# Kernel tuning notes

Measured on AMD Instinct MI355X. Metric: run time of the kernel, lower is better.

The kernel has to match this reference:

```python
import jax, jax.numpy as jnp
import numpy as np

N = 50000
E = 800000
IN_DIM = 128
HID = 128
OUT = 40


def setup_inputs() -> dict:
    key = jax.random.key(0)
    k1, k2, k3, k4, k5 = jax.random.split(key, 5)
    x = jax.random.normal(k1, (N, IN_DIM), dtype=jnp.float32)
    edge_index = jax.random.randint(k2, (2, E), 0, N, dtype=jnp.int64)
    # Glorot-ish init for GCNConv weights, zero bias (PyG default bias=True)
    W1 = jax.random.normal(k3, (IN_DIM, HID), dtype=jnp.float32) / np.sqrt(IN_DIM)
    b1 = jnp.zeros((HID,), dtype=jnp.float32)
    W2 = jax.random.normal(k4, (HID, OUT), dtype=jnp.float32) / np.sqrt(HID)
    b2 = jnp.zeros((OUT,), dtype=jnp.float32)
    return {"x": x, "edge_index": edge_index, "W1": W1, "b1": b1, "W2": W2, "b2": b2}


def _gcn_norm(edge_index, n_nodes):
    """Add self-loops and compute symmetric GCN normalization per edge.
    Returns (src, dst, norm) with len E + n_nodes."""
    loops = jnp.arange(n_nodes, dtype=edge_index.dtype)
    src = jnp.concatenate([edge_index[0], loops])
    dst = jnpp_concat = jnp.concatenate([edge_index[1], loops])
    dst = jnp.concatenate([edge_index[1], loops])
    deg = jax.ops.segment_sum(jnp.ones_like(dst, dtype=jnp.float32), dst,
                              num_segments=n_nodes)
    dinv = jnp.where(deg > 0, jax.lax.rsqrt(deg), 0.0)
    norm = dinv[src] * dinv[dst]  # [E + N]
    return src, dst, norm


def _gcn_conv(x, src, dst, norm, W, b, n_nodes):
    xw = x @ W                                  # [N, F_out] transform first
    msg = xw[src] * norm[:, None]               # gather + scale, [E+N, F_out]
    out = jax.ops.segment_sum(msg, dst, num_segments=n_nodes)  # scatter-add
    return out + b


def reference(x, edge_index, W1, b1, W2, b2):
    n = x.shape[0]
    src, dst, norm = _gcn_norm(edge_index, n)
    h = _gcn_conv(x, src, dst, norm, W1, b1, n)
    h = jax.nn.relu(h)
    # dropout is identity in eval mode (training=False)
    h = _gcn_conv(h, src, dst, norm, W2, b2, n)
    return jax.nn.softmax(h, axis=1)
```

## Files before the change

kernel.cpp:

```cpp
#include <hip/hip_runtime.h>
#include <hip/hip_fp16.h>

#define IN_DIM 128
#define HID    128
#define OUTC   40
#define CAP    64
#define LSTR   136

typedef _Float16 f16x8 __attribute__((ext_vector_type(8)));
typedef _Float16 f16x4 __attribute__((ext_vector_type(4)));
typedef float    f32x4 __attribute__((ext_vector_type(4)));

__device__ __forceinline__ int permi(int d, int NP8) { return (d & 7) * NP8 + (d >> 3); }

__global__ __launch_bounds__(256) void k_scatter(const int* __restrict__ edge, int* __restrict__ cnt,
                                                 int* __restrict__ col,
                                                 const float* __restrict__ W1, const float* __restrict__ W2,
                                                 _Float16* __restrict__ W1T, _Float16* __restrict__ W2T,
                                                 int E, int n, int nbS, int NP8) {
  int b = blockIdx.x;
  if (b >= nbS) {
    int t = (b - nbS) * 256 + threadIdx.x;
    if (t < 128 * 128) {
      int nn = t >> 7, kk = t & 127;
      W1T[t] = (_Float16)W1[kk * 128 + nn];
    }
    if (t < 48 * 128) {
      int nn = t >> 7, kk = t & 127;
      W2T[t] = (nn < OUTC) ? (_Float16)W2[kk * OUTC + nn] : (_Float16)0.f;
    }
    return;
  }
  int g       = b & 7;
  int tid     = (b >> 3) * 256 + threadIdx.x;
  int gstride = (nbS >> 3) * 256;
  for (int e = tid; e < E; e += gstride) {
    int d = edge[E + e];
    if ((unsigned)d >= (unsigned)n || (d & 7) != g) continue;
    int sv = edge[e];
    if ((unsigned)sv >= (unsigned)n) continue;
    int p   = g * NP8 + (d >> 3);
    int pos = atomicAdd(&cnt[p], 1);
    if (pos < CAP) col[(size_t)p * CAP + pos] = sv;
  }
}


__global__ __launch_bounds__(256) void k_gemm1(const float* __restrict__ x, const _Float16* __restrict__ W1T,
                                               const int* __restrict__ cnt, __half* __restrict__ out,
                                               int n, int NP8) {
  __shared__ _Float16 sW[128 * LSTR];
  __shared__ _Float16 sX[64 * LSTR];
  int tid = threadIdx.x;
  int i0  = blockIdx.x * 64;

  {
    const uint4* src = (const uint4*)W1T;
    for (int idx = tid; idx < 2048; idx += 256) {
      int nn = idx >> 4, c = idx & 15;
      *(uint4*)&sW[nn * LSTR + c * 8] = src[nn * 16 + c];
    }
  }
  for (int idx = tid; idx < 2048; idx += 256) {
    int r = idx >> 5, c = idx & 31;
    int row = i0 + r;
    float4 v = (row < n) ? *(const float4*)&x[(size_t)row * IN_DIM + c * 4]
                         : make_float4(0.f, 0.f, 0.f, 0.f);
    f16x4 hv; hv[0] = (_Float16)v.x; hv[1] = (_Float16)v.y; hv[2] = (_Float16)v.z; hv[3] = (_Float16)v.w;
    *(f16x4*)&sX[r * LSTR + c * 4] = hv;
  }
  __syncthreads();

  int wv = tid >> 6, lane = tid & 63;
  int m = lane & 15, quad = lane >> 4;

  const _Float16* ax = &sX[(16 * wv + m) * LSTR + quad * 8];
  f16x8 a0 = *(const f16x8*)(ax);
  f16x8 a1 = *(const f16x8*)(ax + 32);
  f16x8 a2 = *(const f16x8*)(ax + 64);
  f16x8 a3 = *(const f16x8*)(ax + 96);

  int base_row = i0 + 16 * wv + quad * 4;
  float dvr[4];
#pragma unroll
  for (int r = 0; r < 4; ++r) {
    int row = base_row + r;
    dvr[r] = (row < n) ? rsqrtf((float)(cnt[permi(row, NP8)] + 1)) : 0.f;
  }

#pragma unroll
  for (int t = 0; t < 8; ++t) {
    const _Float16* bx = &sW[(t * 16 + m) * LSTR + quad * 8];
    f16x8 b0 = *(const f16x8*)(bx);
    f16x8 b1 = *(const f16x8*)(bx + 32);
    f16x8 b2 = *(const f16x8*)(bx + 64);
    f16x8 b3 = *(const f16x8*)(bx + 96);
    f32x4 c = {0.f, 0.f, 0.f, 0.f};
    c = __builtin_amdgcn_mfma_f32_16x16x32_f16(a0, b0, c, 0, 0, 0);
    c = __builtin_amdgcn_mfma_f32_16x16x32_f16(a1, b1, c, 0, 0, 0);
    c = __builtin_amdgcn_mfma_f32_16x16x32_f16(a2, b2, c, 0, 0, 0);
    c = __builtin_amdgcn_mfma_f32_16x16x32_f16(a3, b3, c, 0, 0, 0);
    int colb = t * 16 + m;
#pragma unroll
    for (int r = 0; r < 4; ++r) {
      int row = base_row + r;
      if (row < n) out[(size_t)row * HID + colb] = __float2half(c[r] * dvr[r]);
    }
  }
}


__global__ __launch_bounds__(256) void k_agg1(const __half2* __restrict__ xws, const int* __restrict__ cnt,
                                              const int* __restrict__ col, const float* __restrict__ b1,
                                              __half2* __restrict__ h, int n, int NP8) {
  int wid  = (blockIdx.x * 256 + threadIdx.x) >> 6;
  int lane = threadIdx.x & 63;
  if (wid >= n) return;
  float2 acc = __half22float2(xws[(size_t)wid * 64 + lane]);
  int p   = permi(wid, NP8);
  int deg = cnt[p];
  int end = min(deg, CAP);
  const int* cp = &col[(size_t)p * CAP];
  int e = 0;
  for (; e + 8 <= end; e += 8) {
    int s0 = cp[e], s1 = cp[e+1], s2 = cp[e+2], s3 = cp[e+3];
    int s4 = cp[e+4], s5 = cp[e+5], s6 = cp[e+6], s7 = cp[e+7];
    float2 v0 = __half22float2(xws[(size_t)s0 * 64 + lane]);
    float2 v1 = __half22float2(xws[(size_t)s1 * 64 + lane]);
    float2 v2 = __half22float2(xws[(size_t)s2 * 64 + lane]);
    float2 v3 = __half22float2(xws[(size_t)s3 * 64 + lane]);
    float2 v4 = __half22float2(xws[(size_t)s4 * 64 + lane]);
    float2 v5 = __half22float2(xws[(size_t)s5 * 64 + lane]);
    float2 v6 = __half22float2(xws[(size_t)s6 * 64 + lane]);
    float2 v7 = __half22float2(xws[(size_t)s7 * 64 + lane]);
    acc.x += (v0.x + v1.x) + (v2.x + v3.x) + ((v4.x + v5.x) + (v6.x + v7.x));
    acc.y += (v0.y + v1.y) + (v2.y + v3.y) + ((v4.y + v5.y) + (v6.y + v7.y));
  }
  for (; e < end; ++e) {
    float2 v = __half22float2(xws[(size_t)cp[e] * 64 + lane]);
    acc.x += v.x; acc.y += v.y;
  }
  float dv = rsqrtf((float)(deg + 1));
  float2 bb = ((const float2*)b1)[lane];
  h[(size_t)wid * 64 + lane] =
      __floats2half2_rn(fmaxf(acc.x * dv + bb.x, 0.f), fmaxf(acc.y * dv + bb.y, 0.f));
}


__global__ __launch_bounds__(256) void k_gemm2(const __half* __restrict__ h, const _Float16* __restrict__ W2T,
                                               const int* __restrict__ cnt, __half* __restrict__ out,
                                               int n, int NP8) {
  __shared__ _Float16 sW[48 * LSTR];
  __shared__ _Float16 sH[64 * LSTR];
  int tid = threadIdx.x;
  int i0  = blockIdx.x * 64;

  {
    const uint4* src = (const uint4*)W2T;
    for (int idx = tid; idx < 768; idx += 256) {
      int nn = idx >> 4, c = idx & 15;
      *(uint4*)&sW[nn * LSTR + c * 8] = src[nn * 16 + c];
    }
  }
  {
    const uint4* src = (const uint4*)h;
    for (int idx = tid; idx < 1024; idx += 256) {
      int r = idx >> 4, c = idx & 15;
      int row = i0 + r;
      uint4 v = (row < n) ? src[(size_t)row * 16 + c] : make_uint4(0u, 0u, 0u, 0u);
      *(uint4*)&sH[r * LSTR + c * 8] = v;
    }
  }
  __syncthreads();

  int wv = tid >> 6, lane = tid & 63;
  int m = lane & 15, quad = lane >> 4;

  const _Float16* ax = &sH[(16 * wv + m) * LSTR + quad * 8];
  f16x8 a0 = *(const f16x8*)(ax);
  f16x8 a1 = *(const f16x8*)(ax + 32);
  f16x8 a2 = *(const f16x8*)(ax + 64);
  f16x8 a3 = *(const f16x8*)(ax + 96);

  int base_row = i0 + 16 * wv + quad * 4;
  float dvr[4];
#pragma unroll
  for (int r = 0; r < 4; ++r) {
    int row = base_row + r;
    dvr[r] = (row < n) ? rsqrtf((float)(cnt[permi(row, NP8)] + 1)) : 0.f;
  }

#pragma unroll
  for (int t = 0; t < 3; ++t) {
    const _Float16* bx = &sW[(t * 16 + m) * LSTR + quad * 8];
    f16x8 b0 = *(const f16x8*)(bx);
    f16x8 b1 = *(const f16x8*)(bx + 32);
    f16x8 b2 = *(const f16x8*)(bx + 64);
    f16x8 b3 = *(const f16x8*)(bx + 96);
    f32x4 c = {0.f, 0.f, 0.f, 0.f};
    c = __builtin_amdgcn_mfma_f32_16x16x32_f16(a0, b0, c, 0, 0, 0);
    c = __builtin_amdgcn_mfma_f32_16x16x32_f16(a1, b1, c, 0, 0, 0);
    c = __builtin_amdgcn_mfma_f32_16x16x32_f16(a2, b2, c, 0, 0, 0);
    c = __builtin_amdgcn_mfma_f32_16x16x32_f16(a3, b3, c, 0, 0, 0);
    int colb = t * 16 + m;
    if (colb < OUTC) {
#pragma unroll
      for (int r = 0; r < 4; ++r) {
        int row = base_row + r;
        if (row < n) out[(size_t)row * OUTC + colb] = __float2half(c[r] * dvr[r]);
      }
    }
  }
}


__global__ __launch_bounds__(256) void k_agg2(const __half* __restrict__ hw, const int* __restrict__ cnt,
                                              const int* __restrict__ col, const float* __restrict__ b2,
                                              float* __restrict__ out, int n, int NP8) {
  int wid  = (blockIdx.x * 256 + threadIdx.x) >> 6;
  int lane = threadIdx.x & 63;
  if (wid >= n) return;
  bool act = lane < OUTC;
  int li = act ? lane : 0;
  float acc = act ? __half2float(hw[(size_t)wid * OUTC + li]) : 0.f;
  int p   = permi(wid, NP8);
  int deg = cnt[p];
  int end = min(deg, CAP);
  const int* cp = &col[(size_t)p * CAP];
  int e = 0;
  for (; e + 8 <= end; e += 8) {
    int s0 = cp[e], s1 = cp[e+1], s2 = cp[e+2], s3 = cp[e+3];
    int s4 = cp[e+4], s5 = cp[e+5], s6 = cp[e+6], s7 = cp[e+7];
    if (act) {
      float a0 = __half2float(hw[(size_t)s0 * OUTC + li]);
      float a1 = __half2float(hw[(size_t)s1 * OUTC + li]);
      float a2 = __half2float(hw[(size_t)s2 * OUTC + li]);
      float a3 = __half2float(hw[(size_t)s3 * OUTC + li]);
      float a4 = __half2float(hw[(size_t)s4 * OUTC + li]);
      float a5 = __half2float(hw[(size_t)s5 * OUTC + li]);
      float a6 = __half2float(hw[(size_t)s6 * OUTC + li]);
      float a7 = __half2float(hw[(size_t)s7 * OUTC + li]);
      acc += (a0 + a1) + (a2 + a3) + ((a4 + a5) + (a6 + a7));
    }
  }
  for (; e < end; ++e) {
    int s = cp[e];
    if (act) acc += __half2float(hw[(size_t)s * OUTC + li]);
  }
  float logit = acc * rsqrtf((float)(deg + 1)) + (act ? b2[lane] : 0.f);
  float m = act ? logit : -1e30f;
#pragma unroll
  for (int o = 32; o > 0; o >>= 1) m = fmaxf(m, __shfl_xor(m, o, 64));
  float ex = act ? __expf(logit - m) : 0.f;
  float sum = ex;
#pragma unroll
  for (int o = 32; o > 0; o >>= 1) sum += __shfl_xor(sum, o, 64);
  if (act) out[(size_t)wid * OUTC + lane] = ex / sum;
}


extern "C" void kernel_launch(void* const* d_in, const int* in_sizes, int n_in,
                              void* d_out, int out_size, void* d_ws, size_t ws_size,
                              hipStream_t stream) {
  const float* x    = (const float*)d_in[0];
  const int*   edge = (const int*)d_in[1];
  const float* W1   = (const float*)d_in[2];
  const float* b1   = (const float*)d_in[3];
  const float* W2   = (const float*)d_in[4];
  const float* b2   = (const float*)d_in[5];
  float* out = (float*)d_out;

  int N   = in_sizes[0] / IN_DIM;
  int E   = in_sizes[1] / 2;
  int NP8 = (N + 7) / 8;
  int NP  = NP8 * 8;

  char* ws = (char*)d_ws;
  size_t off = 0;
  auto carve = [&](size_t bytes) { char* p = ws + off; off = (off + bytes + 255) & ~(size_t)255; return p; };
  int*      cnt = (int*)carve((size_t)NP * 4);
  int*      col = (int*)carve((size_t)NP * CAP * 4);
  _Float16* W1T = (_Float16*)carve((size_t)128 * 128 * 2);
  _Float16* W2T = (_Float16*)carve((size_t)48 * 128 * 2);
  __half*   xws = (__half*)carve((size_t)N * HID * 2);
  __half*   h   = (__half*)carve((size_t)N * HID * 2);
  __half*   hw  = xws;

  hipMemsetAsync(cnt, 0, (size_t)NP * 4, stream);

  int nbS = 1024;
  k_scatter<<<nbS + 64, 256, 0, stream>>>(edge, cnt, col, W1, W2, W1T, W2T, E, N, nbS, NP8);

  k_gemm1<<<(N + 63) / 64, 256, 0, stream>>>(x, W1T, cnt, xws, N, NP8);
  k_agg1<<<(N * 64 + 255) / 256, 256, 0, stream>>>((const __half2*)xws, cnt, col, b1, (__half2*)h, N, NP8);
  k_gemm2<<<(N + 63) / 64, 256, 0, stream>>>(h, W2T, cnt, hw, N, NP8);
  k_agg2<<<(N * 64 + 255) / 256, 256, 0, stream>>>(hw, cnt, col, b2, out, N, NP8);
}
```

Baseline: 220.1 us.

## Two-pass LDS-binned edge partition and 16-bit column indices

Replaces the single scatter kernel, where every block rescanned all edges and kept only one of eight destination groups, with two passes. The first pass bins each edge chunk by destination group in shared memory and flushes contiguous packed (dst>>3, src) words to per-group staging arrays. The second pass scatters from staging into the padded adjacency. Column indices shrink to 16-bit, which halves adjacency traffic in the aggregation kernels but only holds while N fits in 65536 nodes. The change costs an extra kernel launch and a staging buffer round trip.

New measurement: 222.5 us. No clear change (+1.1%).

```diff
diff --git a/kernel.cpp b/kernel.cpp
--- a/kernel.cpp
+++ b/kernel.cpp
@@ -6,6 +6,8 @@
 #define OUTC   40
 #define CAP    64
 #define LSTR   136
+#define CHUNK  4096
+#define BINCAP 800
 
 typedef _Float16 f16x8 __attribute__((ext_vector_type(8)));
 typedef _Float16 f16x4 __attribute__((ext_vector_type(4)));
@@ -13,14 +15,14 @@
 
 __device__ __forceinline__ int permi(int d, int NP8) { return (d & 7) * NP8 + (d >> 3); }
 
-__global__ __launch_bounds__(256) void k_scatter(const int* __restrict__ edge, int* __restrict__ cnt,
-                                                 int* __restrict__ col,
-                                                 const float* __restrict__ W1, const float* __restrict__ W2,
-                                                 _Float16* __restrict__ W1T, _Float16* __restrict__ W2T,
-                                                 int E, int n, int nbS, int NP8) {
+__global__ __launch_bounds__(256) void k_part(const int* __restrict__ edge, unsigned* __restrict__ staging,
+                                              int* __restrict__ gcnt,
+                                              const float* __restrict__ W1, const float* __restrict__ W2,
+                                              _Float16* __restrict__ W1T, _Float16* __restrict__ W2T,
+                                              int E, int n, int nbA, int ES8) {
   int b = blockIdx.x;
-  if (b >= nbS) {
-    int t = (b - nbS) * 256 + threadIdx.x;
+  if (b >= nbA) {
+    int t = (b - nbA) * 256 + threadIdx.x;
     if (t < 128 * 128) {
       int nn = t >> 7, kk = t & 127;
       W1T[t] = (_Float16)W1[kk * 128 + nn];
@@ -31,17 +33,56 @@
     }
     return;
   }
-  int g       = b & 7;
-  int tid     = (b >> 3) * 256 + threadIdx.x;
-  int gstride = (nbS >> 3) * 256;
-  for (int e = tid; e < E; e += gstride) {
-    int d = edge[E + e];
-    if ((unsigned)d >= (unsigned)n || (d & 7) != g) continue;
-    int sv = edge[e];
-    if ((unsigned)sv >= (unsigned)n) continue;
-    int p   = g * NP8 + (d >> 3);
+  __shared__ unsigned lbin[8][BINCAP];
+  __shared__ int lcnt[8];
+  __shared__ int lbase[8];
+  int tid = threadIdx.x;
+  if (tid < 8) lcnt[tid] = 0;
+  __syncthreads();
+  int e0 = b * CHUNK;
+#pragma unroll 4
+  for (int i = 0; i < CHUNK / 256; ++i) {
+    int e = e0 + i * 256 + tid;
+    if (e < E) {
+      int sv = edge[e];
+      int d  = edge[E + e];
+      if ((unsigned)d < (unsigned)n && (unsigned)sv < (unsigned)n) {
+        int g = d & 7;
+        unsigned pk = ((unsigned)(d >> 3) << 16) | (unsigned)sv;
+        int p = atomicAdd(&lcnt[g], 1);
+        if (p < BINCAP) lbin[g][p] = pk;
+        else {
+          int gp = atomicAdd(&gcnt[g], 1);
+          staging[(size_t)g * ES8 + gp] = pk;
+        }
+      }
+    }
+  }
+  __syncthreads();
+  if (tid < 8) lbase[tid] = atomicAdd(&gcnt[tid], min(lcnt[tid], BINCAP));
+  __syncthreads();
+#pragma unroll
+  for (int g = 0; g < 8; ++g) {
+    int c = min(lcnt[g], BINCAP);
+    int base = lbase[g];
+    for (int idx = tid; idx < c; idx += 256)
+      staging[(size_t)g * ES8 + base + idx] = lbin[g][idx];
+  }
+}
+
+__global__ __launch_bounds__(256) void k_scat(const unsigned* __restrict__ staging, const int* __restrict__ gcnt,
+                                              int* __restrict__ cnt, unsigned short* __restrict__ col,
+                                              int NP8, int ES8) {
+  int g = blockIdx.x & 7;
+  int cE = gcnt[g];
+  int t       = (blockIdx.x >> 3) * 256 + threadIdx.x;
+  int gstride = (gridDim.x >> 3) * 256;
+  const unsigned* sg = &staging[(size_t)g * ES8];
+  for (int i = t; i < cE; i += gstride) {
+    unsigned pk = sg[i];
+    int p = g * NP8 + (int)(pk >> 16);
     int pos = atomicAdd(&cnt[p], 1);
-    if (pos < CAP) col[(size_t)p * CAP + pos] = sv;
+    if (pos < CAP) col[(size_t)p * CAP + pos] = (unsigned short)(pk & 0xFFFFu);
   }
 }
 
@@ -111,7 +152,7 @@
 
 
 __global__ __launch_bounds__(256) void k_agg1(const __half2* __restrict__ xws, const int* __restrict__ cnt,
-                                              const int* __restrict__ col, const float* __restrict__ b1,
+                                              const unsigned short* __restrict__ col, const float* __restrict__ b1,
                                               __half2* __restrict__ h, int n, int NP8) {
   int wid  = (blockIdx.x * 256 + threadIdx.x) >> 6;
   int lane = threadIdx.x & 63;
@@ -120,7 +161,7 @@
   int p   = permi(wid, NP8);
   int deg = cnt[p];
   int end = min(deg, CAP);
-  const int* cp = &col[(size_t)p * CAP];
+  const unsigned short* cp = &col[(size_t)p * CAP];
   int e = 0;
   for (; e + 8 <= end; e += 8) {
     int s0 = cp[e], s1 = cp[e+1], s2 = cp[e+2], s3 = cp[e+3];
@@ -215,7 +256,7 @@
 
 
 __global__ __launch_bounds__(256) void k_agg2(const __half* __restrict__ hw, const int* __restrict__ cnt,
-                                              const int* __restrict__ col, const float* __restrict__ b2,
+                                              const unsigned short* __restrict__ col, const float* __restrict__ b2,
                                               float* __restrict__ out, int n, int NP8) {
   int wid  = (blockIdx.x * 256 + threadIdx.x) >> 6;
   int lane = threadIdx.x & 63;
@@ -226,7 +267,7 @@
   int p   = permi(wid, NP8);
   int deg = cnt[p];
   int end = min(deg, CAP);
-  const int* cp = &col[(size_t)p * CAP];
+  const unsigned short* cp = &col[(size_t)p * CAP];
   int e = 0;
   for (; e + 8 <= end; e += 8) {
     int s0 = cp[e], s1 = cp[e+1], s2 = cp[e+2], s3 = cp[e+3];
@@ -274,22 +315,26 @@
   int E   = in_sizes[1] / 2;
   int NP8 = (N + 7) / 8;
   int NP  = NP8 * 8;
+  int ES8 = E / 8 + 16384;
 
   char* ws = (char*)d_ws;
   size_t off = 0;
   auto carve = [&](size_t bytes) { char* p = ws + off; off = (off + bytes + 255) & ~(size_t)255; return p; };
-  int*      cnt = (int*)carve((size_t)NP * 4);
-  int*      col = (int*)carve((size_t)NP * CAP * 4);
-  _Float16* W1T = (_Float16*)carve((size_t)128 * 128 * 2);
-  _Float16* W2T = (_Float16*)carve((size_t)48 * 128 * 2);
-  __half*   xws = (__half*)carve((size_t)N * HID * 2);
-  __half*   h   = (__half*)carve((size_t)N * HID * 2);
-  __half*   hw  = xws;
-
-  hipMemsetAsync(cnt, 0, (size_t)NP * 4, stream);
-
-  int nbS = 1024;
-  k_scatter<<<nbS + 64, 256, 0, stream>>>(edge, cnt, col, W1, W2, W1T, W2T, E, N, nbS, NP8);
+  int*            gcnt    = (int*)carve(8 * 4);
+  int*            cnt     = (int*)carve((size_t)NP * 4);
+  unsigned*       staging = (unsigned*)carve((size_t)8 * ES8 * 4);
+  unsigned short* col     = (unsigned short*)carve((size_t)NP * CAP * 2);
+  _Float16*       W1T     = (_Float16*)carve((size_t)128 * 128 * 2);
+  _Float16*       W2T     = (_Float16*)carve((size_t)48 * 128 * 2);
+  __half*         xws     = (__half*)carve((size_t)N * HID * 2);
+  __half*         h       = (__half*)carve((size_t)N * HID * 2);
+  __half*         hw      = xws;
+
+  hipMemsetAsync(gcnt, 0, (size_t)((char*)staging - (char*)gcnt), stream);
+
+  int nbA = (E + CHUNK - 1) / CHUNK;
+  k_part<<<nbA + 64, 256, 0, stream>>>(edge, staging, gcnt, W1, W2, W1T, W2T, E, N, nbA, ES8);
+  k_scat<<<512, 256, 0, stream>>>(staging, gcnt, cnt, col, NP8, ES8);
 
   k_gemm1<<<(N + 63) / 64, 256, 0, stream>>>(x, W1T, cnt, xws, N, NP8);
   k_agg1<<<(N * 64 + 255) / 256, 256, 0, stream>>>((const __half2*)xws, cnt, col, b1, (__half2*)h, N, NP8);
```

## Split degree count from scatter and co-schedule scatter with first GEMM

Applied to the files above, without the earlier changes.

Degree counting moves into a separate prep kernel, so the first GEMM (which needs degrees for normalization) can run in the same launch as the column-list scatter, overlapping atomic-bound scatter work with MFMA work. Column indices are stored as 16-bit values to halve index traffic in both aggregations. The second aggregation now uses half2 loads and float2 stores across 20 lanes. This adds an extra kernel and a second counter array, and the 16-bit indices only hold for graphs with fewer than 65536 nodes.

Result: slower. 278.6 us (+26.6%).

```diff
diff --git a/kernel.cpp b/kernel.cpp
--- a/kernel.cpp
+++ b/kernel.cpp
@@ -13,46 +13,61 @@
 
 __device__ __forceinline__ int permi(int d, int NP8) { return (d & 7) * NP8 + (d >> 3); }
 
-__global__ __launch_bounds__(256) void k_scatter(const int* __restrict__ edge, int* __restrict__ cnt,
-                                                 int* __restrict__ col,
-                                                 const float* __restrict__ W1, const float* __restrict__ W2,
-                                                 _Float16* __restrict__ W1T, _Float16* __restrict__ W2T,
-                                                 int E, int n, int nbS, int NP8) {
+__global__ __launch_bounds__(256) void k_prep(const int* __restrict__ edge, int* __restrict__ cnt,
+                                              const float* __restrict__ W1, const float* __restrict__ W2,
+                                              _Float16* __restrict__ W1T, _Float16* __restrict__ W2T,
+                                              int E, int n, int nbC, int NP8) {
   int b = blockIdx.x;
-  if (b >= nbS) {
-    int t = (b - nbS) * 256 + threadIdx.x;
-    if (t < 128 * 128) {
-      int nn = t >> 7, kk = t & 127;
-      W1T[t] = (_Float16)W1[kk * 128 + nn];
-    }
-    if (t < 48 * 128) {
-      int nn = t >> 7, kk = t & 127;
-      W2T[t] = (nn < OUTC) ? (_Float16)W2[kk * OUTC + nn] : (_Float16)0.f;
+  if (b < nbC) {
+    int e      = b * 256 + threadIdx.x;
+    int stride = nbC * 256;
+    for (; e < E; e += stride) {
+      int d = __builtin_nontemporal_load(&edge[E + e]);
+      if ((unsigned)d < (unsigned)n) atomicAdd(&cnt[permi(d, NP8)], 1);
     }
     return;
   }
-  int g       = b & 7;
-  int tid     = (b >> 3) * 256 + threadIdx.x;
-  int gstride = (nbS >> 3) * 256;
-  for (int e = tid; e < E; e += gstride) {
-    int d = edge[E + e];
-    if ((unsigned)d >= (unsigned)n || (d & 7) != g) continue;
-    int sv = edge[e];
-    if ((unsigned)sv >= (unsigned)n) continue;
-    int p   = g * NP8 + (d >> 3);
-    int pos = atomicAdd(&cnt[p], 1);
-    if (pos < CAP) col[(size_t)p * CAP + pos] = sv;
-  }
-}
-
-
-__global__ __launch_bounds__(256) void k_gemm1(const float* __restrict__ x, const _Float16* __restrict__ W1T,
-                                               const int* __restrict__ cnt, __half* __restrict__ out,
-                                               int n, int NP8) {
-  __shared__ _Float16 sW[128 * LSTR];
-  __shared__ _Float16 sX[64 * LSTR];
+  int t = (b - nbC) * 256 + threadIdx.x;
+  if (t < 128 * 128) {
+    int nn = t >> 7, kk = t & 127;
+    W1T[t] = (_Float16)W1[kk * 128 + nn];
+  }
+  if (t < 48 * 128) {
+    int nn = t >> 7, kk = t & 127;
+    W2T[t] = (nn < OUTC) ? (_Float16)W2[kk * OUTC + nn] : (_Float16)0.f;
+  }
+}
+
+#define SMEM_SZ (128 * LSTR * 2 + 64 * LSTR * 2)
+
+__global__ __launch_bounds__(256) void k_scatter_gemm1(const int* __restrict__ edge, int* __restrict__ fill,
+                                                       unsigned short* __restrict__ col,
+                                                       const float* __restrict__ x, const _Float16* __restrict__ W1T,
+                                                       const int* __restrict__ cnt, __half* __restrict__ xws,
+                                                       int E, int n, int nbS, int NP8) {
+  __shared__ __align__(16) char smem[SMEM_SZ];
+  int b   = blockIdx.x;
   int tid = threadIdx.x;
-  int i0  = blockIdx.x * 64;
+
+  if (b < nbS) {
+    int g       = b & 7;
+    int t       = (b >> 3) * 256 + tid;
+    int gstride = (nbS >> 3) * 256;
+    for (int e = t; e < E; e += gstride) {
+      int d = __builtin_nontemporal_load(&edge[E + e]);
+      if ((unsigned)d >= (unsigned)n || (d & 7) != g) continue;
+      int sv = __builtin_nontemporal_load(&edge[e]);
+      if ((unsigned)sv >= (unsigned)n) continue;
+      int p   = g * NP8 + (d >> 3);
+      int pos = atomicAdd(&fill[p], 1);
+      if (pos < CAP) col[(size_t)p * CAP + pos] = (unsigned short)sv;
+    }
+    return;
+  }
+
+  _Float16* sW = (_Float16*)smem;
+  _Float16* sX = (_Float16*)(smem + 128 * LSTR * 2);
+  int i0 = (b - nbS) * 64;
 
   {
     const uint4* src = (const uint4*)W1T;
@@ -104,14 +119,14 @@
 #pragma unroll
     for (int r = 0; r < 4; ++r) {
       int row = base_row + r;
-      if (row < n) out[(size_t)row * HID + colb] = __float2half(c[r] * dvr[r]);
+      if (row < n) xws[(size_t)row * HID + colb] = __float2half(c[r] * dvr[r]);
     }
   }
 }
 
 
 __global__ __launch_bounds__(256) void k_agg1(const __half2* __restrict__ xws, const int* __restrict__ cnt,
-                                              const int* __restrict__ col, const float* __restrict__ b1,
+                                              const unsigned short* __restrict__ col, const float* __restrict__ b1,
                                               __half2* __restrict__ h, int n, int NP8) {
   int wid  = (blockIdx.x * 256 + threadIdx.x) >> 6;
   int lane = threadIdx.x & 63;
@@ -120,7 +135,7 @@
   int p   = permi(wid, NP8);
   int deg = cnt[p];
   int end = min(deg, CAP);
-  const int* cp = &col[(size_t)p * CAP];
+  const unsigned short* cp = &col[(size_t)p * CAP];
   int e = 0;
   for (; e + 8 <= end; e += 8) {
     int s0 = cp[e], s1 = cp[e+1], s2 = cp[e+2], s3 = cp[e+3];
@@ -214,48 +229,60 @@
 }
 
 
-__global__ __launch_bounds__(256) void k_agg2(const __half* __restrict__ hw, const int* __restrict__ cnt,
-                                              const int* __restrict__ col, const float* __restrict__ b2,
+__global__ __launch_bounds__(256) void k_agg2(const __half2* __restrict__ hw2, const int* __restrict__ cnt,
+                                              const unsigned short* __restrict__ col, const float* __restrict__ b2,
                                               float* __restrict__ out, int n, int NP8) {
   int wid  = (blockIdx.x * 256 + threadIdx.x) >> 6;
   int lane = threadIdx.x & 63;
   if (wid >= n) return;
-  bool act = lane < OUTC;
+  bool act = lane < (OUTC / 2);
   int li = act ? lane : 0;
-  float acc = act ? __half2float(hw[(size_t)wid * OUTC + li]) : 0.f;
+  float2 acc = __half22float2(hw2[(size_t)wid * (OUTC / 2) + li]);
+  if (!act) { acc.x = 0.f; acc.y = 0.f; }
   int p   = permi(wid, NP8);
   int deg = cnt[p];
   int end = min(deg, CAP);
-  const int* cp = &col[(size_t)p * CAP];
+  const unsigned short* cp = &col[(size_t)p * CAP];
   int e = 0;
   for (; e + 8 <= end; e += 8) {
     int s0 = cp[e], s1 = cp[e+1], s2 = cp[e+2], s3 = cp[e+3];
     int s4 = cp[e+4], s5 = cp[e+5], s6 = cp[e+6], s7 = cp[e+7];
     if (act) {
-      float a0 = __half2float(hw[(size_t)s0 * OUTC + li]);
-      float a1 = __half2float(hw[(size_t)s1 * OUTC + li]);
-      float a2 = __half2float(hw[(size_t)s2 * OUTC + li]);
-      float a3 = __half2float(hw[(size_t)s3 * OUTC + li]);
-      float a4 = __half2float(hw[(size_t)s4 * OUTC + li]);
-      float a5 = __half2float(hw[(size_t)s5 * OUTC + li]);
-      float a6 = __half2float(hw[(size_t)s6 * OUTC + li]);
-      float a7 = __half2float(hw[(size_t)s7 * OUTC + li]);
-      acc += (a0 + a1) + (a2 + a3) + ((a4 + a5) + (a6 + a7));
+      float2 v0 = __half22float2(hw2[(size_t)s0 * (OUTC / 2) + li]);
+      float2 v1 = __half22float2(hw2[(size_t)s1 * (OUTC / 2) + li]);
+      float2 v2 = __half22float2(hw2[(size_t)s2 * (OUTC / 2) + li]);
+      float2 v3 = __half22float2(hw2[(size_t)s3 * (OUTC / 2) + li]);
+      float2 v4 = __half22float2(hw2[(size_t)s4 * (OUTC / 2) + li]);
+      float2 v5 = __half22float2(hw2[(size_t)s5 * (OUTC / 2) + li]);
+      float2 v6 = __half22float2(hw2[(size_t)s6 * (OUTC / 2) + li]);
+      float2 v7 = __half22float2(hw2[(size_t)s7 * (OUTC / 2) + li]);
+      acc.x += (v0.x + v1.x) + (v2.x + v3.x) + ((v4.x + v5.x) + (v6.x + v7.x));
+      acc.y += (v0.y + v1.y) + (v2.y + v3.y) + ((v4.y + v5.y) + (v6.y + v7.y));
     }
   }
   for (; e < end; ++e) {
     int s = cp[e];
-    if (act) acc += __half2float(hw[(size_t)s * OUTC + li]);
-  }
-  float logit = acc * rsqrtf((float)(deg + 1)) + (act ? b2[lane] : 0.f);
-  float m = act ? logit : -1e30f;
+    if (act) {
+      float2 v = __half22float2(hw2[(size_t)s * (OUTC / 2) + li]);
+      acc.x += v.x; acc.y += v.y;
+    }
+  }
+  float dvd = rsqrtf((float)(deg + 1));
+  float2 bb = act ? ((const float2*)b2)[lane] : make_float2(0.f, 0.f);
+  float lx = acc.x * dvd + bb.x;
+  float ly = acc.y * dvd + bb.y;
+  float m = act ? fmaxf(lx, ly) : -1e30f;
 #pragma unroll
   for (int o = 32; o > 0; o >>= 1) m = fmaxf(m, __shfl_xor(m, o, 64));
-  float ex = act ? __expf(logit - m) : 0.f;
-  float sum = ex;
+  float ex = act ? __expf(lx - m) : 0.f;
+  float ey = act ? __expf(ly - m) : 0.f;
+  float sum = ex + ey;
 #pragma unroll
   for (int o = 32; o > 0; o >>= 1) sum += __shfl_xor(sum, o, 64);
-  if (act) out[(size_t)wid * OUTC + lane] = ex / sum;
+  if (act) {
+    float inv = 1.f / sum;
+    ((float2*)out)[(size_t)wid * (OUTC / 2) + lane] = make_float2(ex * inv, ey * inv);
+  }
 }
 
 
@@ -278,21 +305,24 @@
   char* ws = (char*)d_ws;
   size_t off = 0;
   auto carve = [&](size_t bytes) { char* p = ws + off; off = (off + bytes + 255) & ~(size_t)255; return p; };
-  int*      cnt = (int*)carve((size_t)NP * 4);
-  int*      col = (int*)carve((size_t)NP * CAP * 4);
-  _Float16* W1T = (_Float16*)carve((size_t)128 * 128 * 2);
-  _Float16* W2T = (_Float16*)carve((size_t)48 * 128 * 2);
-  __half*   xws = (__half*)carve((size_t)N * HID * 2);
-  __half*   h   = (__half*)carve((size_t)N * HID * 2);
-  __half*   hw  = xws;
-
-  hipMemsetAsync(cnt, 0, (size_t)NP * 4, stream);
-
+  int*            cnt  = (int*)carve((size_t)NP * 4);
+  int*            fill = (int*)carve((size_t)NP * 4);
+  unsigned short* col  = (unsigned short*)carve((size_t)NP * CAP * 2);
+  _Float16*       W1T  = (_Float16*)carve((size_t)128 * 128 * 2);
+  _Float16*       W2T  = (_Float16*)carve((size_t)48 * 128 * 2);
+  __half*         xws  = (__half*)carve((size_t)N * HID * 2);
+  __half*         h    = (__half*)carve((size_t)N * HID * 2);
+  __half*         hw   = xws;
+
+  hipMemsetAsync(cnt, 0, (size_t)((char*)col - (char*)cnt), stream);
+
+  int nbC = 1024;
   int nbS = 1024;
-  k_scatter<<<nbS + 64, 256, 0, stream>>>(edge, cnt, col, W1, W2, W1T, W2T, E, N, nbS, NP8);
-
-  k_gemm1<<<(N + 63) / 64, 256, 0, stream>>>(x, W1T, cnt, xws, N, NP8);
+  int nbG = (N + 63) / 64;
+
+  k_prep<<<nbC + 64, 256, 0, stream>>>(edge, cnt, W1, W2, W1T, W2T, E, N, nbC, NP8);
+  k_scatter_gemm1<<<nbS + nbG, 256, 0, stream>>>(edge, fill, col, x, W1T, cnt, xws, E, N, nbS, NP8);
   k_agg1<<<(N * 64 + 255) / 256, 256, 0, stream>>>((const __half2*)xws, cnt, col, b1, (__half2*)h, N, NP8);
-  k_gemm2<<<(N + 63) / 64, 256, 0, stream>>>(h, W2T, cnt, hw, N, NP8);
-  k_agg2<<<(N * 64 + 255) / 256, 256, 0, stream>>>(hw, cnt, col, b2, out, N, NP8);
-}
+  k_gemm2<<<nbG, 256, 0, stream>>>(h, W2T, cnt, hw, N, NP8);
+  k_agg2<<<(N * 64 + 255) / 256, 256, 0, stream>>>((const __half2*)hw, cnt, col, b2, out, N, NP8);
+}
```
